# Performance work log

Measured on AMD Instinct MI355X. Metric: run time of the kernel, lower is better.

The kernel has to match this reference:

```python
import jax, jax.numpy as jnp
import numpy as np

N_NODES = 100000
N_EDGES = 400000
B = 1024
D_XD = 78
SEQ = 1000
EMB = 128
HID = 300
NF = 32
OUT_DIM = 128


def setup_inputs():
    key = jax.random.key(0)
    ks = jax.random.split(key, 40)
    rn = lambda k, s, sc=0.05: jax.random.normal(k, s, dtype=jnp.float32) * sc
    inp = {}
    inp['x'] = rn(ks[0], (N_NODES, D_XD), 1.0)
    inp['edge_index'] = jax.random.randint(ks[1], (2, N_EDGES), 0, N_NODES, dtype=jnp.int32)
    inp['batch'] = jnp.sort(jax.random.randint(ks[2], (N_NODES,), 0, B, dtype=jnp.int32))
    inp['target'] = jax.random.randint(ks[3], (B, SEQ), 0, 26, dtype=jnp.int32)
    inp['embs'] = rn(ks[4], (B * 13, 133), 1.0)
    inp['W1'] = rn(ks[5], (D_XD, D_XD)); inp['b1'] = jnp.zeros((D_XD,), jnp.float32)
    inp['W2'] = rn(ks[6], (D_XD, D_XD * 2)); inp['b2'] = jnp.zeros((D_XD * 2,), jnp.float32)
    inp['W3'] = rn(ks[7], (D_XD * 2, D_XD * 4)); inp['b3'] = jnp.zeros((D_XD * 4,), jnp.float32)
    inp['fc_g1_w'] = rn(ks[8], (D_XD * 4, 1024)); inp['fc_g1_b'] = jnp.zeros((1024,), jnp.float32)
    inp['fc_g2_w'] = rn(ks[9], (1024, OUT_DIM)); inp['fc_g2_b'] = jnp.zeros((OUT_DIM,), jnp.float32)
    inp['emb_xt'] = rn(ks[10], (26, EMB), 1.0)
    inp['conv_w'] = rn(ks[11], (NF, SEQ, 8)); inp['conv_b'] = jnp.zeros((NF,), jnp.float32)
    inp['fc1xt_w'] = rn(ks[12], (NF * 121, OUT_DIM)); inp['fc1xt_b'] = jnp.zeros((OUT_DIM,), jnp.float32)
    inp['fg_lin_w'] = rn(ks[13], (133, HID)); inp['fg_lin_b'] = jnp.zeros((HID,), jnp.float32)
    inp['Wq'] = rn(ks[14], (HID, HID)); inp['Wk'] = rn(ks[15], (HID, HID)); inp['Wv'] = rn(ks[16], (HID, HID))
    inp['ln_g'] = jnp.ones((HID,), jnp.float32); inp['ln_b'] = jnp.zeros((HID,), jnp.float32)
    inp['fg_out_w'] = rn(ks[17], (HID, OUT_DIM)); inp['fg_out_b'] = jnp.zeros((OUT_DIM,), jnp.float32)
    inp['fc1_w'] = rn(ks[18], (3 * OUT_DIM, 1024)); inp['fc1_b'] = jnp.zeros((1024,), jnp.float32)
    inp['fc2_w'] = rn(ks[19], (1024, 512)); inp['fc2_b'] = jnp.zeros((512,), jnp.float32)
    inp['out_w'] = rn(ks[20], (512, 1)); inp['out_b'] = jnp.zeros((1,), jnp.float32)
    return inp


def _gcn_conv(h_in, W, b, src, dst, dis):
    # PyG GCNConv: x' = D^-1/2 (A+I) D^-1/2 (X W) + b
    h = h_in @ W
    norm = dis[src] * dis[dst]  # [E]
    agg = jax.ops.segment_sum(h[src] * norm[:, None], dst, num_segments=h.shape[0])
    agg = agg + h * (dis * dis)[:, None]  # self-loop term
    return agg + b


def _forward(x, embs, W1, b1, W2, b2, W3, b3, fc_g1_w, fc_g1_b, fc_g2_w, fc_g2_b,
             emb_xt, conv_w, conv_b, fc1xt_w, fc1xt_b, fg_lin_w, fg_lin_b,
             Wq, Wk, Wv, ln_g, ln_b, fg_out_w, fg_out_b,
             fc1_w, fc1_b, fc2_w, fc2_b, out_w, out_b,
             edge_index, batch, target):
    src, dst = edge_index[0], edge_index[1]
    deg = jax.ops.segment_sum(jnp.ones_like(dst, jnp.float32), dst, num_segments=x.shape[0]) + 1.0
    dis = jax.lax.rsqrt(deg)
    h = jax.nn.relu(_gcn_conv(x, W1, b1, src, dst, dis))
    h = jax.nn.relu(_gcn_conv(h, W2, b2, src, dst, dis))
    h = jax.nn.relu(_gcn_conv(h, W3, b3, src, dst, dis))
    g = jax.ops.segment_max(h, batch, num_segments=B)  # global max pool
    g = jnp.where(jnp.isfinite(g), g, 0.0)
    g = jax.nn.relu(g @ fc_g1_w + fc_g1_b)
    g = g @ fc_g2_w + fc_g2_b  # dropout is identity at eval
    # protein branch: embedding + Conv1d(in=1000, out=32, k=8) over embed axis
    e = emb_xt[target]  # [B, SEQ, EMB]
    c = jax.lax.conv_general_dilated(e, conv_w, (1,), 'VALID',
                                     dimension_numbers=('NCH', 'OIH', 'NCH'))
    c = c + conv_b[None, :, None]  # [B, 32, 121]
    xt = c.reshape(B, NF * 121) @ fc1xt_w + fc1xt_b
    # functional-group prompt branch (KANO-style): linear -> self-attn -> LN -> gather row i*13
    f = (embs @ fg_lin_w + fg_lin_b).reshape(B, 13, HID)
    q = f @ Wq; k = f @ Wk; v = f @ Wv
    attn = jax.nn.softmax(jnp.einsum('bqd,bkd->bqk', q, k) / jnp.sqrt(jnp.float32(HID)), axis=-1)
    f2 = f + jnp.einsum('bqk,bkd->bqd', attn, v)
    mu = f2.mean(-1, keepdims=True)
    var = f2.var(-1, keepdims=True)
    f2 = (f2 - mu) * jax.lax.rsqrt(var + 1e-5) * ln_g + ln_b
    fg = f2[:, 0, :] @ fg_out_w + fg_out_b  # row i*13 per molecule
    xc = jnp.concatenate([g, xt, fg], axis=1)  # [B, 3*OUT_DIM]
    xc = jax.nn.relu(xc @ fc1_w + fc1_b)
    xc = jax.nn.relu(xc @ fc2_w + fc2_b)
    return xc @ out_w + out_b


def reference(x, edge_index, batch, target, embs, W1, b1, W2, b2, W3, b3,
              fc_g1_w, fc_g1_b, fc_g2_w, fc_g2_b, emb_xt, conv_w, conv_b,
              fc1xt_w, fc1xt_b, fg_lin_w, fg_lin_b, Wq, Wk, Wv, ln_g, ln_b,
              fg_out_w, fg_out_b, fc1_w, fc1_b, fc2_w, fc2_b, out_w, out_b):
    return _forward(x, embs, W1, b1, W2, b2, W3, b3, fc_g1_w, fc_g1_b, fc_g2_w, fc_g2_b,
                    emb_xt, conv_w, conv_b, fc1xt_w, fc1xt_b, fg_lin_w, fg_lin_b,
                    Wq, Wk, Wv, ln_g, ln_b, fg_out_w, fg_out_b,
                    fc1_w, fc1_b, fc2_w, fc2_b, out_w, out_b,
                    edge_index, batch, target)
```

## Files before the change

### kernel.cpp

```cpp
#include <hip/hip_runtime.h>
#include <hip/hip_bf16.h>
#include <math.h>

#define NNODES 100000
#define NEDGES 400000
#define NB     1024
#define SEQ    1000
#define HID    300
#define NBLK1  ((NNODES + 255) / 256)

typedef __attribute__((ext_vector_type(8))) short short8;
typedef __attribute__((ext_vector_type(4))) float f32x4;

__device__ __forceinline__ float bf_lo(unsigned int v) { return __uint_as_float(v << 16); }
__device__ __forceinline__ float bf_hi(unsigned int v) { return __uint_as_float(v & 0xffff0000u); }
__device__ __forceinline__ unsigned int bf_pack(float lo, float hi) {
    __hip_bfloat16 a = __float2bfloat16(lo), b = __float2bfloat16(hi);
    unsigned short ua = *(unsigned short*)&a, ub = *(unsigned short*)&b;
    return (unsigned int)ua | ((unsigned int)ub << 16);
}

__global__ void cvt_pad_kernel(const float* __restrict__ in, __hip_bfloat16* __restrict__ out,
                               int M, int K, int Kpad)
{
    long idx = (long)blockIdx.x * 256 + threadIdx.x;
    if (idx >= (long)M * Kpad) return;
    int m = idx / Kpad, k = idx % Kpad;
    out[idx] = __float2bfloat16(k < K ? in[(long)m * K + k] : 0.f);
}

__global__ void transpose_cvt_kernel(const float* __restrict__ in, __hip_bfloat16* __restrict__ out,
                                     int K, int N, int Kpad)
{
    long idx = (long)blockIdx.x * 256 + threadIdx.x;
    if (idx >= (long)N * Kpad) return;
    int n = idx / Kpad, k = idx % Kpad;
    out[idx] = __float2bfloat16(k < K ? in[(long)k * N + n] : 0.f);
}

struct TBatch {
    const float* src[12];
    __hip_bfloat16* dst[12];
    int K[12]; int N[12]; int Kpad[12];
    int bstart[13];
};

__global__ __launch_bounds__(256) void transpose_batch_kernel(TBatch tb)
{
    int blk = blockIdx.x;
    int d = 0;
    while (d < 11 && blk >= tb.bstart[d + 1]) ++d;
    long idx = (long)(blk - tb.bstart[d]) * 256 + threadIdx.x;
    long tot = (long)tb.N[d] * tb.Kpad[d];
    if (idx >= tot) return;
    int Kpad = tb.Kpad[d];
    int n = idx / Kpad, k = idx % Kpad;
    tb.dst[d][idx] = __float2bfloat16(k < tb.K[d] ? tb.src[d][(long)k * tb.N[d] + n] : 0.f);
}

__global__ __launch_bounds__(256) void gemm_bf16_kernel(
    const __hip_bfloat16* __restrict__ A, const __hip_bfloat16* __restrict__ Bt,
    const float* __restrict__ bias, void* __restrict__ C,
    int M, int N, int Kpad, int lda, int ldc, int Npad_out,
    int relu, int outbf, int chunk)
{
    __shared__ __align__(16) __hip_bfloat16 As[64][40];
    __shared__ __align__(16) __hip_bfloat16 Bs[64][40];
    int tid = threadIdx.x;
    int wave = tid >> 6, lane = tid & 63;
    int wm = wave >> 1, wn = wave & 1;
    int quad = lane >> 4, l16 = lane & 15;
    int row0 = blockIdx.y * 64, col0 = blockIdx.x * 64;

    int kbeg = 0, kend = Kpad;
    if (chunk > 0) { kbeg = blockIdx.z * chunk; kend = kbeg + chunk; if (kend > Kpad) kend = Kpad; }

    f32x4 acc[2][2];
    #pragma unroll
    for (int i = 0; i < 2; ++i)
        #pragma unroll
        for (int j = 0; j < 2; ++j) acc[i][j] = (f32x4){0.f, 0.f, 0.f, 0.f};

    int r = tid >> 2, cch = (tid & 3) * 8;

    for (int k0 = kbeg; k0 < kend; k0 += 32) {
        uint4 av = {0u, 0u, 0u, 0u};
        if (row0 + r < M) av = *(const uint4*)(A + (size_t)(row0 + r) * lda + k0 + cch);
        *(uint4*)(&As[r][cch]) = av;
        uint4 bv = {0u, 0u, 0u, 0u};
        if (col0 + r < N) bv = *(const uint4*)(Bt + (size_t)(col0 + r) * Kpad + k0 + cch);
        *(uint4*)(&Bs[r][cch]) = bv;
        __syncthreads();

        short8 a0 = *(const short8*)(&As[wm * 32 + l16][quad * 8]);
        short8 a1 = *(const short8*)(&As[wm * 32 + 16 + l16][quad * 8]);
        short8 b0 = *(const short8*)(&Bs[wn * 32 + l16][quad * 8]);
        short8 b1 = *(const short8*)(&Bs[wn * 32 + 16 + l16][quad * 8]);
        acc[0][0] = __builtin_amdgcn_mfma_f32_16x16x32_bf16(a0, b0, acc[0][0], 0, 0, 0);
        acc[0][1] = __builtin_amdgcn_mfma_f32_16x16x32_bf16(a0, b1, acc[0][1], 0, 0, 0);
        acc[1][0] = __builtin_amdgcn_mfma_f32_16x16x32_bf16(a1, b0, acc[1][0], 0, 0, 0);
        acc[1][1] = __builtin_amdgcn_mfma_f32_16x16x32_bf16(a1, b1, acc[1][1], 0, 0, 0);
        __syncthreads();
    }

    #pragma unroll
    for (int ti = 0; ti < 2; ++ti) {
        int rbase = row0 + wm * 32 + ti * 16 + quad * 4;
        #pragma unroll
        for (int tj = 0; tj < 2; ++tj) {
            int cc = col0 + wn * 32 + tj * 16 + l16;
            if (cc >= Npad_out) continue;
            #pragma unroll
            for (int reg = 0; reg < 4; ++reg) {
                int rr = rbase + reg;
                if (rr >= M) continue;
                float v = acc[ti][tj][reg];
                if (chunk > 0) {
                    if (cc < N) atomicAdd((float*)C + (size_t)rr * ldc + cc, v);
                } else {
                    float ov = 0.f;
                    if (cc < N) {
                        if (bias) v += bias[cc];
                        if (relu) v = fmaxf(v, 0.f);
                        ov = v;
                    }
                    if (outbf) ((__hip_bfloat16*)C)[(size_t)rr * ldc + cc] = __float2bfloat16(ov);
                    else       ((float*)C)[(size_t)rr * ldc + cc] = ov;
                }
            }
        }
    }
}

static void launch_gemm_bf16(const __hip_bfloat16* A, const __hip_bfloat16* Bt, const float* bias,
                             void* C, int M, int N, int Kpad, int lda, int ldc, int Npad_out,
                             int relu, int outbf, int splitz, hipStream_t stream)
{
    int cover = N > Npad_out ? N : Npad_out;
    int chunk = (splitz > 1) ? (Kpad / splitz) : 0;
    dim3 grid((cover + 63) / 64, (M + 63) / 64, splitz > 1 ? splitz : 1);
    gemm_bf16_kernel<<<grid, 256, 0, stream>>>(A, Bt, bias, C, M, N, Kpad, lda, ldc, Npad_out,
                                               relu, outbf, chunk);
}

__global__ __launch_bounds__(256) void gemm_big_kernel(
    const __hip_bfloat16* __restrict__ A, const __hip_bfloat16* __restrict__ Bt,
    const float* __restrict__ bias, __hip_bfloat16* __restrict__ C,
    int M, int N, int Kpad, int lda, int ldc, int Npad_out)
{
    __shared__ __align__(16) __hip_bfloat16 As[128][40];
    __shared__ __align__(16) __hip_bfloat16 Bs[64][40];
    int tid = threadIdx.x;
    int wave = tid >> 6, lane = tid & 63;
    int wm = wave >> 1, wn = wave & 1;
    int quad = lane >> 4, l16 = lane & 15;
    int row0 = blockIdx.y * 128, col0 = blockIdx.x * 64;

    f32x4 acc[4][2];
    #pragma unroll
    for (int i = 0; i < 4; ++i)
        #pragma unroll
        for (int j = 0; j < 2; ++j) acc[i][j] = (f32x4){0.f, 0.f, 0.f, 0.f};

    int r = tid >> 2, cch = (tid & 3) * 8;

    for (int k0 = 0; k0 < Kpad; k0 += 32) {
        uint4 av0 = {0u, 0u, 0u, 0u}, av1 = {0u, 0u, 0u, 0u}, bv = {0u, 0u, 0u, 0u};
        if (row0 + r < M)      av0 = *(const uint4*)(A + (size_t)(row0 + r) * lda + k0 + cch);
        if (row0 + r + 64 < M) av1 = *(const uint4*)(A + (size_t)(row0 + r + 64) * lda + k0 + cch);
        if (col0 + r < N)      bv  = *(const uint4*)(Bt + (size_t)(col0 + r) * Kpad + k0 + cch);
        *(uint4*)(&As[r][cch]) = av0;
        *(uint4*)(&As[r + 64][cch]) = av1;
        *(uint4*)(&Bs[r][cch]) = bv;
        __syncthreads();

        short8 af[4], bféin[2];
        #pragma unroll
        for (int i = 0; i < 4; ++i)
            af[i] = *(const short8*)(&As[wm * 64 + i * 16 + l16][quad * 8]);
        #pragma unroll
        for (int j = 0; j < 2; ++j)
            bféin[j] = *(const short8*)(&Bs[wn * 32 + j * 16 + l16][quad * 8]);
        #pragma unroll
        for (int i = 0; i < 4; ++i)
            #pragma unroll
            for (int j = 0; j < 2; ++j)
                acc[i][j] = __builtin_amdgcn_mfma_f32_16x16x32_bf16(af[i], bféin[j], acc[i][j], 0, 0, 0);
        __syncthreads();
    }

    #pragma unroll
    for (int ti = 0; ti < 4; ++ti) {
        int rbase = row0 + wm * 64 + ti * 16 + quad * 4;
        #pragma unroll
        for (int tj = 0; tj < 2; ++tj) {
            int cc = col0 + wn * 32 + tj * 16 + l16;
            if (cc >= Npad_out) continue;
            #pragma unroll
            for (int reg = 0; reg < 4; ++reg) {
                int rr = rbase + reg;
                if (rr >= M) continue;
                float v = acc[ti][tj][reg];
                float ov = 0.f;
                if (cc < N) ov = fmaxf(v + bias[cc], 0.f);
                C[(size_t)rr * ldc + cc] = __float2bfloat16(ov);
            }
        }
    }
}

static void launch_gemm_big(const __hip_bfloat16* A, const __hip_bfloat16* Bt, const float* bias,
                            __hip_bfloat16* C, int M, int N, int Kpad, int lda, int ldc,
                            int Npad_out, hipStream_t stream)
{
    int cover = N > Npad_out ? N : Npad_out;
    dim3 grid((cover + 63) / 64, (M + 127) / 128);
    gemm_big_kernel<<<grid, 256, 0, stream>>>(A, Bt, bias, C, M, N, Kpad, lda, ldc, Npad_out);
}

__global__ void deg_kernel(const int* __restrict__ dst, int* __restrict__ deg, int E)
{
    int e = blockIdx.x * 256 + threadIdx.x;
    if (e < E) atomicAdd(&deg[dst[e]], 1);
}

__global__ void dis_kernel(const int* __restrict__ deg, float* __restrict__ dis,
                           float* __restrict__ selfc, int n)
{
    int i = blockIdx.x * 256 + threadIdx.x;
    if (i < n) {
        float d = (float)deg[i] + 1.0f;
        float r = 1.0f / sqrtf(d);
        dis[i] = r;
        selfc[i] = r * r;
    }
}

__global__ __launch_bounds__(256) void scan_p1(const int* __restrict__ deg,
                                               int* __restrict__ off, int* __restrict__ bsum)
{
    __shared__ int s[256];
    int tid = threadIdx.x;
    int i = blockIdx.x * 256 + tid;
    int v = (i < NNODES) ? deg[i] : 0;
    s[tid] = v;
    __syncthreads();
    #pragma unroll
    for (int d = 1; d < 256; d <<= 1) {
        int t = (tid >= d) ? s[tid - d] : 0;
        __syncthreads();
        s[tid] += t;
        __syncthreads();
    }
    if (i < NNODES) off[i] = s[tid] - v;
    if (tid == 255) bsum[blockIdx.x] = s[255];
}

__global__ __launch_bounds__(512) void scan_p2(int* __restrict__ bsum)
{
    __shared__ int s[512];
    int tid = threadIdx.x;
    int v = (tid < NBLK1) ? bsum[tid] : 0;
    s[tid] = v;
    __syncthreads();
    #pragma unroll
    for (int d = 1; d < 512; d <<= 1) {
        int t = (tid >= d) ? s[tid - d] : 0;
        __syncthreads();
        s[tid] += t;
        __syncthreads();
    }
    if (tid < NBLK1) bsum[tid] = s[tid] - v;
}

__global__ __launch_bounds__(256) void scan_p3(int* __restrict__ off, const int* __restrict__ bsum,
                                               int* __restrict__ cur)
{
    int i = blockIdx.x * 256 + threadIdx.x;
    if (i < NNODES) {
        int v = off[i] + bsum[blockIdx.x];
        off[i] = v;
        cur[i] = v;
    }
    if (i == NNODES) off[NNODES] = NEDGES;
}

__global__ void fill_csr_kernel(const int* __restrict__ src, const int* __restrict__ dst,
                                const float* __restrict__ dis, int* __restrict__ cur,
                                int* __restrict__ csr_src, float* __restrict__ csr_w, int E)
{
    int e = blockIdx.x * 256 + threadIdx.x;
    if (e >= E) return;
    int s = src[e], d = dst[e];
    int p = atomicAdd(&cur[d], 1);
    csr_src[p] = s;
    csr_w[p] = dis[s] * dis[d];
}

__global__ __launch_bounds__(256) void gcn_agg2(
    const __hip_bfloat16* __restrict__ Tin, const int* __restrict__ off,
    const int* __restrict__ csr_src, const float* __restrict__ csr_w,
    const float* __restrict__ selfc, __hip_bfloat16* __restrict__ out,
    int half, int nc)
{
    int wave = threadIdx.x >> 6, lane = threadIdx.x & 63;
    int node = blockIdx.x * 4 + wave;
    if (node >= NNODES) return;
    const unsigned int* Tp = (const unsigned int*)Tin;
    unsigned int* Op = (unsigned int*)out;
    size_t rb = (size_t)node * half;
    bool m0 = lane < half;
    bool m1 = (nc > 1) && (lane + 64 < half);
    float sc = selfc[node];
    float a0x = 0.f, a0y = 0.f, a1x = 0.f, a1y = 0.f;
    float b0x = 0.f, b0y = 0.f, b1x = 0.f, b1y = 0.f;
    if (m0) { unsigned int v = Tp[rb + lane];      a0x = bf_lo(v) * sc; a0y = bf_hi(v) * sc; }
    if (m1) { unsigned int v = Tp[rb + lane + 64]; a1x = bf_lo(v) * sc; a1y = bf_hi(v) * sc; }
    int s0 = off[node], s1 = off[node + 1];
    int e = s0;
    for (; e + 2 <= s1; e += 2) {
        int i0 = csr_src[e], i1 = csr_src[e + 1];
        float w0 = csr_w[e], w1 = csr_w[e + 1];
        size_t p0 = (size_t)i0 * half, p1 = (size_t)i1 * half;
        unsigned int v00 = 0u, v01 = 0u, v10 = 0u, v11 = 0u;
        if (m0) { v00 = Tp[p0 + lane]; v10 = Tp[p1 + lane]; }
        if (m1) { v01 = Tp[p0 + lane + 64]; v11 = Tp[p1 + lane + 64]; }
        if (m0) {
            a0x += bf_lo(v00) * w0; a0y += bf_hi(v00) * w0;
            b0x += bf_lo(v10) * w1; b0y += bf_hi(v10) * w1;
        }
        if (m1) {
            a1x += bf_lo(v01) * w0; a1y += bf_hi(v01) * w0;
            b1x += bf_lo(v11) * w1; b1y += bf_hi(v11) * w1;
        }
    }
    if (e < s1) {
        int i0 = csr_src[e];
        float w0 = csr_w[e];
        size_t p0 = (size_t)i0 * half;
        if (m0) { unsigned int v = Tp[p0 + lane];      a0x += bf_lo(v) * w0; a0y += bf_hi(v) * w0; }
        if (m1) { unsigned int v = Tp[p0 + lane + 64]; a1x += bf_lo(v) * w0; a1y += bf_hi(v) * w0; }
    }
    if (m0) Op[rb + lane]      = bf_pack(a0x + b0x, a0y + b0y);
    if (m1) Op[rb + lane + 64] = bf_pack(a1x + b1x, a1y + b1y);
}

__global__ __launch_bounds__(256) void pool_max_bf16(
    const __hip_bfloat16* __restrict__ H, const int* __restrict__ batch,
    __hip_bfloat16* __restrict__ g)
{
    int b = blockIdx.x;
    int lo = 0, hi = NNODES;
    while (lo < hi) { int mid = (lo + hi) >> 1; if (batch[mid] < b) lo = mid + 1; else hi = mid; }
    int s = lo;
    hi = NNODES;
    while (lo < hi) { int mid = (lo + hi) >> 1; if (batch[mid] < b + 1) lo = mid + 1; else hi = mid; }
    int e = lo;
    int tid = threadIdx.x;
    if (tid < 160) {
        const unsigned int* Hp = (const unsigned int*)H;
        float mx = 0.f, my = 0.f;
        for (int i = s; i < e; ++i) {
            unsigned int v = Hp[(size_t)i * 160 + tid];
            mx = fmaxf(mx, bf_lo(v));
            my = fmaxf(my, bf_hi(v));
        }
        ((unsigned int*)g)[(size_t)b * 160 + tid] = bf_pack(mx, my);
    }
}

__global__ void conv_transpose_kernel(const float* __restrict__ w, __hip_bfloat16* __restrict__ wt)
{
    int idx = blockIdx.x * 256 + threadIdx.x;
    if (idx >= 256000) return;
    int o = idx / 8000;
    int rem = idx - o * 8000;
    int i = rem >> 3, k = rem & 7;
    wt[i * 256 + o * 8 + k] = __float2bfloat16(w[idx]);
}

__global__ __launch_bounds__(256) void conv_agg_kernel(
    const __hip_bfloat16* __restrict__ cwt, const int* __restrict__ target,
    __hip_bfloat16* __restrict__ aggw)
{
    __shared__ int tb_s[SEQ];
    __shared__ int cnt[26];
    __shared__ int boff[27];
    __shared__ int curs[26];
    __shared__ int bucket[SEQ];
    __shared__ float comb[3][256];
    int b = blockIdx.x, tid = threadIdx.x;
    int wave = tid >> 6, lane = tid & 63;
    const int* tb = target + b * SEQ;
    if (tid < 26) cnt[tid] = 0;
    __syncthreads();
    for (int i = tid; i < SEQ; i += 256) {
        int a = tb[i];
        tb_s[i] = a;
        atomicAdd(&cnt[a], 1);
    }
    __syncthreads();
    if (tid == 0) {
        int run = 0;
        for (int a = 0; a < 26; ++a) { boff[a] = run; curs[a] = run; run += cnt[a]; }
        boff[26] = run;
    }
    __syncthreads();
    for (int i = tid; i < SEQ; i += 256) {
        int a = tb_s[i];
        int p = atomicAdd(&curs[a], 1);
        bucket[p] = i;
    }
    __syncthreads();

    const uint2* cw = (const uint2*)cwt;
    uint2* aw = (uint2*)aggw;
    for (int a = 0; a < 26; ++a) {
        int s = boff[a], e = boff[a + 1];
        float x0 = 0.f, x1 = 0.f, x2 = 0.f, x3 = 0.f;
        float y0 = 0.f, y1 = 0.f, y2 = 0.f, y3 = 0.f;
        int j = s + wave;
        for (; j + 4 < e; j += 8) {
            uint2 v = cw[(size_t)bucket[j] * 64 + lane];
            uint2 u = cw[(size_t)bucket[j + 4] * 64 + lane];
            x0 += bf_lo(v.x); x1 += bf_hi(v.x); x2 += bf_lo(v.y); x3 += bf_hi(v.y);
            y0 += bf_lo(u.x); y1 += bf_hi(u.x); y2 += bf_lo(u.y); y3 += bf_hi(u.y);
        }
        if (j < e) {
            uint2 v = cw[(size_t)bucket[j] * 64 + lane];
            x0 += bf_lo(v.x); x1 += bf_hi(v.x); x2 += bf_lo(v.y); x3 += bf_hi(v.y);
        }
        x0 += y0; x1 += y1; x2 += y2; x3 += y3;
        if (wave > 0) {
            comb[wave - 1][lane * 4 + 0] = x0;
            comb[wave - 1][lane * 4 + 1] = x1;
            comb[wave - 1][lane * 4 + 2] = x2;
            comb[wave - 1][lane * 4 + 3] = x3;
        }
        __syncthreads();
        if (wave == 0) {
            x0 += comb[0][lane * 4 + 0] + comb[1][lane * 4 + 0] + comb[2][lane * 4 + 0];
            x1 += comb[0][lane * 4 + 1] + comb[1][lane * 4 + 1] + comb[2][lane * 4 + 1];
            x2 += comb[0][lane * 4 + 2] + comb[1][lane * 4 + 2] + comb[2][lane * 4 + 2];
            x3 += comb[0][lane * 4 + 3] + comb[1][lane * 4 + 3] + comb[2][lane * 4 + 3];
            uint2 o;
            o.x = bf_pack(x0, x1);
            o.y = bf_pack(x2, x3);
            aw[(size_t)b * 1664 + a * 64 + lane] = o;
        }
        __syncthreads();
    }
}

__global__ __launch_bounds__(128) void conv_wc_kernel(
    const float* __restrict__ emb, const float* __restrict__ w_fc, float* __restrict__ Wc)
{
    int o = blockIdx.x;
    int ak = blockIdx.y;
    int a = ak >> 3, k = ak & 7;
    int j = threadIdx.x;
    const float* wp = w_fc + (long)(o * 121) * 128 + j;
    const float* ep = emb + a * 128 + k;
    float s = 0.f;
    #pragma unroll 11
    for (int t = 0; t < 121; ++t) s += ep[t] * wp[t * 128];
    Wc[(long)(a * 256 + o * 8 + k) * 128 + j] = s;
}

__global__ void xtb_init_kernel(const float* __restrict__ b_fc, float* __restrict__ xtb)
{
    xtb[threadIdx.x] = b_fc[threadIdx.x];
}

__global__ __launch_bounds__(128) void convb_fold_kernel(
    const float* __restrict__ w_fc, const float* __restrict__ conv_b, float* __restrict__ xtb)
{
    int o = blockIdx.x, j = threadIdx.x;
    const float* wp = w_fc + (long)(o * 121) * 128 + j;
    float s = 0.f;
    for (int t = 0; t < 121; ++t) s += wp[t * 128];
    atomicAdd(&xtb[j], s * conv_b[o]);
}

__global__ void xc_convbias_kernel(const float* __restrict__ xtb, float* __restrict__ xc)
{
    int idx = blockIdx.x * 256 + threadIdx.x;
    if (idx >= NB * 128) return;
    int b = idx >> 7, j = idx & 127;
    xc[(long)b * 384 + 128 + j] = xtb[j];
}

__global__ __launch_bounds__(256) void attn_ln_kernel(
    const __hip_bfloat16* __restrict__ Fb, const __hip_bfloat16* __restrict__ Kf,
    const __hip_bfloat16* __restrict__ Vf, const __hip_bfloat16* __restrict__ q0,
    const float* __restrict__ ln_g, const float* __restrict__ ln_b,
    __hip_bfloat16* __restrict__ out)
{
    int b = blockIdx.x, tid = threadIdx.x;
    __shared__ float qs[HID];
    __shared__ float sc[13];
    __shared__ float red[256];
    __shared__ float red2[256];
    __shared__ float rowv[HID];
    __shared__ float mean_s, inv_s;

    for (int d = tid; d < HID; d += 256) qs[d] = __bfloat162float(q0[(size_t)b * 320 + d]);
    __syncthreads();
    if (tid < 208) {
        int k = tid >> 4, sub = tid & 15;
        const __hip_bfloat16* kr = Kf + ((size_t)b * 13 + k) * 320;
        float p = 0.f;
        for (int d = sub; d < HID; d += 16) p += qs[d] * __bfloat162float(kr[d]);
        red[tid] = p;
    }
    __syncthreads();
    if (tid < 208 && (tid & 15) == 0) {
        float s = 0.f;
        #pragma unroll
        for (int j = 0; j < 16; ++j) s += red[tid + j];
        sc[tid >> 4] = s * 0.0577350269189626f;
    }
    __syncthreads();
    if (tid == 0) {
        float mx = sc[0];
        for (int k = 1; k < 13; ++k) mx = fmaxf(mx, sc[k]);
        float ssum = 0.f;
        for (int k = 0; k < 13; ++k) { float e = expf(sc[k] - mx); sc[k] = e; ssum += e; }
        float inv = 1.0f / ssum;
        for (int k = 0; k < 13; ++k) sc[k] *= inv;
    }
    __syncthreads();
    for (int d = tid; d < HID; d += 256) {
        float v = __bfloat162float(Fb[((size_t)b * 13) * 320 + d]);
        #pragma unroll
        for (int k = 0; k < 13; ++k)
            v += sc[k] * __bfloat162float(Vf[((size_t)b * 13 + k) * 320 + d]);
        rowv[d] = v;
    }
    __syncthreads();
    float s1 = 0.f, s2 = 0.f;
    for (int d = tid; d < HID; d += 256) { float v = rowv[d]; s1 += v; s2 += v * v; }
    red[tid] = s1; red2[tid] = s2;
    __syncthreads();
    for (int s = 128; s > 0; s >>= 1) {
        if (tid < s) { red[tid] += red[tid + s]; red2[tid] += red2[tid + s]; }
        __syncthreads();
    }
    if (tid == 0) {
        float mean = red[0] / (float)HID;
        float var = red2[0] / (float)HID - mean * mean;
        mean_s = mean;
        inv_s = 1.0f / sqrtf(var + 1e-5f);
    }
    __syncthreads();
    for (int d = tid; d < 320; d += 256) {
        float v = 0.f;
        if (d < HID) v = (rowv[d] - mean_s) * inv_s * ln_g[d] + ln_b[d];
        out[(size_t)b * 320 + d] = __float2bfloat16(v);
    }
}

__global__ __launch_bounds__(256) void final_out_kernel(
    const float* __restrict__ X, const float* __restrict__ w,
    const float* __restrict__ bias, float* __restrict__ out)
{
    int b = blockIdx.x, tid = threadIdx.x;
    __shared__ float red[256];
    float p = X[(long)b * 512 + tid] * w[tid] + X[(long)b * 512 + tid + 256] * w[tid + 256];
    red[tid] = p;
    __syncthreads();
    for (int s = 128; s > 0; s >>= 1) {
        if (tid < s) red[tid] += red[tid + s];
        __syncthreads();
    }
    if (tid == 0) out[b] = red[0] + bias[0];
}

extern "C" void kernel_launch(void* const* d_in, const int* in_sizes, int n_in,
                              void* d_out, int out_size, void* d_ws, size_t ws_size,
                              hipStream_t stream)
{
    const float* x        = (const float*)d_in[0];
    const int*   ei       = (const int*)d_in[1];
    const int*   batch    = (const int*)d_in[2];
    const int*   target   = (const int*)d_in[3];
    const float* embs     = (const float*)d_in[4];
    const float* W1       = (const float*)d_in[5];
    const float* b1       = (const float*)d_in[6];
    const float* W2       = (const float*)d_in[7];
    const float* b2       = (const float*)d_in[8];
    const float* W3       = (const float*)d_in[9];
    const float* b3       = (const float*)d_in[10];
    const float* fc_g1_w  = (const float*)d_in[11];
    const float* fc_g1_b  = (const float*)d_in[12];
    const float* fc_g2_w  = (const float*)d_in[13];
    const float* fc_g2_b  = (const float*)d_in[14];
    const float* emb_xt   = (const float*)d_in[15];
    const float* conv_w   = (const float*)d_in[16];
    const float* conv_b   = (const float*)d_in[17];
    const float* fc1xt_w  = (const float*)d_in[18];
    const float* fc1xt_b  = (const float*)d_in[19];
    const float* fg_lin_w = (const float*)d_in[20];
    const float* fg_lin_b = (const float*)d_in[21];
    const float* Wq       = (const float*)d_in[22];
    const float* Wk       = (const float*)d_in[23];
    const float* Wv       = (const float*)d_in[24];
    const float* ln_g     = (const float*)d_in[25];
    const float* ln_b     = (const float*)d_in[26];
    const float* fg_out_w = (const float*)d_in[27];
    const float* fg_out_b = (const float*)d_in[28];
    const float* fc1_w    = (const float*)d_in[29];
    const float* fc1_b    = (const float*)d_in[30];
    const float* fc2_w    = (const float*)d_in[31];
    const float* fc2_b    = (const float*)d_in[32];
    const float* out_w    = (const float*)d_in[33];
    const float* out_b    = (const float*)d_in[34];

    const int* src = ei;
    const int* dst = ei + NEDGES;
    typedef __hip_bfloat16 bf;

    char* p = (char*)d_ws;
    auto alloc = [&](size_t bytes) { char* r = p; p += (bytes + 255) & ~(size_t)255; return r; };
    bf*   xb      = (bf*)alloc((size_t)NNODES * 96 * 2);
    bf*   T       = (bf*)alloc((size_t)NNODES * 160 * 2);
    bf*   H       = (bf*)alloc((size_t)NNODES * 320 * 2);
    int*  deg     = (int*)alloc(NNODES * 4);
    float* dis    = (float*)alloc(NNODES * 4);
    float* selfc  = (float*)alloc(NNODES * 4);
    int*  off     = (int*)alloc((NNODES + 1) * 4);
    int*  bsum    = (int*)alloc(512 * 4);
    int*  csr_src = (int*)alloc(NEDGES * 4);
    float* csr_w  = (float*)alloc(NEDGES * 4);
    bf*   w1t     = (bf*)alloc(78 * 96 * 2);
    bf*   w2t     = (bf*)alloc(156 * 96 * 2);
    bf*   w3t     = (bf*)alloc(312 * 160 * 2);
    bf*   fcg1t   = (bf*)alloc(1024 * 320 * 2);
    bf*   fcg2t   = (bf*)alloc(128 * 1024 * 2);
    bf*   fglint  = (bf*)alloc(300 * 160 * 2);
    bf*   wkt     = (bf*)alloc(300 * 320 * 2);
    bf*   wvt     = (bf*)alloc(300 * 320 * 2);
    bf*   wqt     = (bf*)alloc(300 * 320 * 2);
    bf*   fgoutt  = (bf*)alloc(128 * 320 * 2);
    bf*   fc1t    = (bf*)alloc(1024 * 384 * 2);
    bf*   fc2t    = (bf*)alloc(512 * 1024 * 2);
    bf*   g       = (bf*)alloc((size_t)NB * 320 * 2);
    bf*   G1b     = (bf*)alloc((size_t)NB * 1024 * 2);
    bf*   embsb   = (bf*)alloc((size_t)NB * 13 * 160 * 2);
    bf*   Fbuf    = (bf*)alloc((size_t)NB * 13 * 320 * 2);
    bf*   Kbuf    = (bf*)alloc((size_t)NB * 13 * 320 * 2);
    bf*   Vbuf    = (bf*)alloc((size_t)NB * 13 * 320 * 2);
    bf*   Qbuf    = (bf*)alloc((size_t)NB * 320 * 2);
    bf*   f2row   = (bf*)alloc((size_t)NB * 320 * 2);
    float* xc     = (float*)alloc((size_t)NB * 384 * 4);
    bf*   xcb     = (bf*)alloc((size_t)NB * 384 * 2);
    float* F2     = (float*)alloc((size_t)NB * 512 * 4);
    bf*   cwt     = (bf*)alloc(256000 * 2);
    bf*   aggwb   = (bf*)alloc((size_t)NB * 6656 * 2);
    float* Wc     = (float*)alloc((size_t)6656 * 128 * 4);
    bf*   Wct     = (bf*)alloc((size_t)128 * 6656 * 2);
    float* xtb    = (float*)alloc(128 * 4);

    hipMemsetAsync(deg, 0, NNODES * sizeof(int), stream);
    deg_kernel<<<(NEDGES + 255) / 256, 256, 0, stream>>>(dst, deg, NEDGES);
    dis_kernel<<<(NNODES + 255) / 256, 256, 0, stream>>>(deg, dis, selfc, NNODES);
    scan_p1<<<NBLK1, 256, 0, stream>>>(deg, off, bsum);
    scan_p2<<<1, 512, 0, stream>>>(bsum);
    scan_p3<<<NBLK1, 256, 0, stream>>>(off, bsum, deg);
    fill_csr_kernel<<<(NEDGES + 255) / 256, 256, 0, stream>>>(src, dst, dis, deg, csr_src, csr_w, NEDGES);

    {
        TBatch tb;
        const float* srcs[12] = {W1, W2, W3, fc_g1_w, fc_g2_w, fg_lin_w, Wk, Wv, Wq, fg_out_w, fc1_w, fc2_w};
        bf* dsts[12]          = {w1t, w2t, w3t, fcg1t, fcg2t, fglint, wkt, wvt, wqt, fgoutt, fc1t, fc2t};
        int Ks[12]    = {78, 78, 156, 312, 1024, 133, 300, 300, 300, 300, 384, 1024};
        int Ns[12]    = {78, 156, 312, 1024, 128, 300, 300, 300, 300, 128, 1024, 512};
        int Kpads[12] = {96, 96, 160, 320, 1024, 160, 320, 320, 320, 320, 384, 1024};
        int bs = 0;
        for (int i = 0; i < 12; ++i) {
            tb.src[i] = srcs[i]; tb.dst[i] = dsts[i];
            tb.K[i] = Ks[i]; tb.N[i] = Ns[i]; tb.Kpad[i] = Kpads[i];
            tb.bstart[i] = bs;
            bs += (int)(((long)Ns[i] * Kpads[i] + 255) / 256);
        }
        tb.bstart[12] = bs;
        transpose_batch_kernel<<<bs, 256, 0, stream>>>(tb);
    }
    cvt_pad_kernel<<<((long)NNODES * 96 + 255) / 256, 256, 0, stream>>>(x, xb, NNODES, 78, 96);
    cvt_pad_kernel<<<((long)NB * 13 * 160 + 255) / 256, 256, 0, stream>>>(embs, embsb, NB * 13, 133, 160);

    int agrid = (NNODES + 3) / 4;
    gcn_agg2<<<agrid, 256, 0, stream>>>(xb, off, csr_src, csr_w, selfc, T, 48, 1);
    launch_gemm_big(T, w1t, b1, H, NNODES, 78, 96, 96, 96, 96, stream);

    gcn_agg2<<<agrid, 256, 0, stream>>>(H, off, csr_src, csr_w, selfc, T, 48, 1);
    launch_gemm_big(T, w2t, b2, H, NNODES, 156, 96, 96, 160, 160, stream);

    gcn_agg2<<<agrid, 256, 0, stream>>>(H, off, csr_src, csr_w, selfc, T, 80, 2);
    launch_gemm_big(T, w3t, b3, H, NNODES, 312, 160, 160, 320, 320, stream);

    pool_max_bf16<<<NB, 256, 0, stream>>>(H, batch, g);
    launch_gemm_bf16(g, fcg1t, fc_g1_b, G1b, NB, 1024, 320, 320, 1024, 1024, 1, 1, 1, stream);
    launch_gemm_bf16(G1b, fcg2t, fc_g2_b, xc, NB, 128, 1024, 1024, 384, 128, 0, 0, 1, stream);

    conv_transpose_kernel<<<(256000 + 255) / 256, 256, 0, stream>>>(conv_w, cwt);
    conv_agg_kernel<<<NB, 256, 0, stream>>>(cwt, target, aggwb);
    conv_wc_kernel<<<dim3(32, 208), 128, 0, stream>>>(emb_xt, fc1xt_w, Wc);
    transpose_cvt_kernel<<<((long)128 * 6656 + 255) / 256, 256, 0, stream>>>(Wc, Wct, 6656, 128, 6656);
    xtb_init_kernel<<<1, 128, 0, stream>>>(fc1xt_b, xtb);
    convb_fold_kernel<<<32, 128, 0, stream>>>(fc1xt_w, conv_b, xtb);
    xc_convbias_kernel<<<(NB * 128 + 255) / 256, 256, 0, stream>>>(xtb, xc);
    launch_gemm_bf16(aggwb, Wct, nullptr, xc + 128, NB, 128, 6656, 6656, 384, 128, 0, 0, 8, stream);

    launch_gemm_bf16(embsb, fglint, fg_lin_b, Fbuf, NB * 13, 300, 160, 160, 320, 320, 0, 1, 1, stream);
    launch_gemm_bf16(Fbuf, wkt, nullptr, Kbuf, NB * 13, 300, 320, 320, 320, 320, 0, 1, 1, stream);
    launch_gemm_bf16(Fbuf, wvt, nullptr, Vbuf, NB * 13, 300, 320, 320, 320, 320, 0, 1, 1, stream);
    launch_gemm_bf16(Fbuf, wqt, nullptr, Qbuf, NB, 300, 320, 13 * 320, 320, 320, 0, 1, 1, stream);
    attn_ln_kernel<<<NB, 256, 0, stream>>>(Fbuf, Kbuf, Vbuf, Qbuf, ln_g, ln_b, f2row);
    launch_gemm_bf16(f2row, fgoutt, fg_out_b, xc + 256, NB, 128, 320, 320, 384, 128, 0, 0, 1, stream);

    cvt_pad_kernel<<<((long)NB * 384 + 255) / 256, 256, 0, stream>>>(xc, xcb, NB, 384, 384);
    launch_gemm_bf16(xcb, fc1t, fc1_b, G1b, NB, 1024, 384, 384, 1024, 1024, 1, 1, 1, stream);
    launch_gemm_bf16(G1b, fc2t, fc2_b, F2, NB, 512, 1024, 1024, 512, 512, 1, 0, 1, stream);
    final_out_kernel<<<NB, 256, 0, stream>>>(F2, out_w, out_b, (float*)d_out);
}
```

Measured before the change: 760.0 us.

## Fold fg_lin into Q/K/V weights, add strip GEMM, unroll GCN aggregation

Three separate changes. First, the fg_lin weight is precomposed with Wq, Wk and Wv, and the bias is folded in, so Q, K and V are computed directly from the 160-wide embeddings instead of chaining off the 320-wide F. Second, the GCN dense layers get a new strip GEMM that loads a 128-row A tile into LDS once and loops over every output column tile, reading B from global memory. Third, the edge aggregation loop is unrolled by four with four accumulator sets to raise memory-level parallelism. This adds small weight-precompose GEMMs to every call, rounds the composed weights to bf16, and may lower occupancy because of the large LDS tile.

```diff
diff --git a/kernel.cpp b/kernel.cpp
--- a/kernel.cpp
+++ b/kernel.cpp
@@ -56,6 +56,16 @@
     int Kpad = tb.Kpad[d];
     int n = idx / Kpad, k = idx % Kpad;
     tb.dst[d][idx] = __float2bfloat16(k < tb.K[d] ? tb.src[d][(long)k * tb.N[d] + n] : 0.f);
+}
+
+__global__ void bias_fold_kernel(const float* __restrict__ b, const float* __restrict__ W,
+                                 float* __restrict__ out, int K, int N)
+{
+    int n = blockIdx.x * 256 + threadIdx.x;
+    if (n >= N) return;
+    float s = 0.f;
+    for (int k = 0; k < K; ++k) s += b[k] * W[(size_t)k * N + n];
+    out[n] = s;
 }
 
 __global__ __launch_bounds__(256) void gemm_bf16_kernel(
@@ -143,10 +153,10 @@
                                                relu, outbf, chunk);
 }
 
-__global__ __launch_bounds__(256) void gemm_big_kernel(
+__global__ __launch_bounds__(256) void gemm_mt_kernel(
     const __hip_bfloat16* __restrict__ A, const __hip_bfloat16* __restrict__ Bt,
     const float* __restrict__ bias, __hip_bfloat16* __restrict__ C,
-    int M, int N, int Kpad, int lda, int ldc, int Npad_out)
+    int M, int N, int Kpad, int lda, int ldc, int Npad_out, int relu)
 {
     __shared__ __align__(16) __hip_bfloat16 As[128][40];
     __shared__ __align__(16) __hip_bfloat16 Bs[64][40];
@@ -174,18 +184,18 @@
         *(uint4*)(&Bs[r][cch]) = bv;
         __syncthreads();
 
-        short8 af[4], bféin[2];
+        short8 af[4], bfr[2];
         #pragma unroll
         for (int i = 0; i < 4; ++i)
             af[i] = *(const short8*)(&As[wm * 64 + i * 16 + l16][quad * 8]);
         #pragma unroll
         for (int j = 0; j < 2; ++j)
-            bféin[j] = *(const short8*)(&Bs[wn * 32 + j * 16 + l16][quad * 8]);
+            bfr[j] = *(const short8*)(&Bs[wn * 32 + j * 16 + l16][quad * 8]);
         #pragma unroll
         for (int i = 0; i < 4; ++i)
             #pragma unroll
             for (int j = 0; j < 2; ++j)
-                acc[i][j] = __builtin_amdgcn_mfma_f32_16x16x32_bf16(af[i], bféin[j], acc[i][j], 0, 0, 0);
+                acc[i][j] = __builtin_amdgcn_mfma_f32_16x16x32_bf16(af[i], bfr[j], acc[i][j], 0, 0, 0);
         __syncthreads();
     }
 
@@ -202,20 +212,100 @@
                 if (rr >= M) continue;
                 float v = acc[ti][tj][reg];
                 float ov = 0.f;
-                if (cc < N) ov = fmaxf(v + bias[cc], 0.f);
+                if (cc < N) {
+                    if (bias) v += bias[cc];
+                    if (relu) v = fmaxf(v, 0.f);
+                    ov = v;
+                }
                 C[(size_t)rr * ldc + cc] = __float2bfloat16(ov);
             }
         }
     }
 }
 
-static void launch_gemm_big(const __hip_bfloat16* A, const __hip_bfloat16* Bt, const float* bias,
-                            __hip_bfloat16* C, int M, int N, int Kpad, int lda, int ldc,
-                            int Npad_out, hipStream_t stream)
+static void launch_gemm_mt(const __hip_bfloat16* A, const __hip_bfloat16* Bt, const float* bias,
+                           __hip_bfloat16* C, int M, int N, int Kpad, int lda, int ldc,
+                           int Npad_out, int relu, hipStream_t stream)
 {
     int cover = N > Npad_out ? N : Npad_out;
     dim3 grid((cover + 63) / 64, (M + 127) / 128);
-    gemm_big_kernel<<<grid, 256, 0, stream>>>(A, Bt, bias, C, M, N, Kpad, lda, ldc, Npad_out);
+    gemm_mt_kernel<<<grid, 256, 0, stream>>>(A, Bt, bias, C, M, N, Kpad, lda, ldc, Npad_out, relu);
+}
+
+__global__ __launch_bounds__(256) void gemm_strip_kernel(
+    const __hip_bfloat16* __restrict__ A, const __hip_bfloat16* __restrict__ Bt,
+    const float* __restrict__ bias, __hip_bfloat16* __restrict__ C,
+    int M, int N, int Kpad, int lda, int ldc, int Npad_out)
+{
+    __shared__ __align__(16) __hip_bfloat16 As[128][168];
+    int tid = threadIdx.x;
+    int wave = tid >> 6, lane = tid & 63;
+    int wm = wave >> 1, wn = wave & 1;
+    int quad = lane >> 4, l16 = lane & 15;
+    int row0 = blockIdx.x * 128;
+
+    int nch = Kpad >> 3;
+    for (int idx = tid; idx < 128 * nch; idx += 256) {
+        int rr = idx / nch, ch = idx - rr * nch;
+        uint4 v = {0u, 0u, 0u, 0u};
+        if (row0 + rr < M) v = *(const uint4*)(A + (size_t)(row0 + rr) * lda + ch * 8);
+        *(uint4*)(&As[rr][ch * 8]) = v;
+    }
+    __syncthreads();
+
+    const short8 bz = {0, 0, 0, 0, 0, 0, 0, 0};
+    int nct = (Npad_out + 63) >> 6;
+    for (int ct = 0; ct < nct; ++ct) {
+        int col0 = ct * 64;
+        f32x4 acc[4][2];
+        #pragma unroll
+        for (int i = 0; i < 4; ++i)
+            #pragma unroll
+            for (int j = 0; j < 2; ++j) acc[i][j] = (f32x4){0.f, 0.f, 0.f, 0.f};
+
+        for (int k0 = 0; k0 < Kpad; k0 += 32) {
+            short8 af[4], bfr[2];
+            #pragma unroll
+            for (int i = 0; i < 4; ++i)
+                af[i] = *(const short8*)(&As[wm * 64 + i * 16 + l16][k0 + quad * 8]);
+            #pragma unroll
+            for (int j = 0; j < 2; ++j) {
+                int cb = col0 + wn * 32 + j * 16 + l16;
+                bfr[j] = (cb < N) ? *(const short8*)(Bt + (size_t)cb * Kpad + k0 + quad * 8) : bz;
+            }
+            #pragma unroll
+            for (int i = 0; i < 4; ++i)
+                #pragma unroll
+                for (int j = 0; j < 2; ++j)
+                    acc[i][j] = __builtin_amdgcn_mfma_f32_16x16x32_bf16(af[i], bfr[j], acc[i][j], 0, 0, 0);
+        }
+
+        #pragma unroll
+        for (int ti = 0; ti < 4; ++ti) {
+            int rbase = row0 + wm * 64 + ti * 16 + quad * 4;
+            #pragma unroll
+            for (int tj = 0; tj < 2; ++tj) {
+                int cc = col0 + wn * 32 + tj * 16 + l16;
+                if (cc >= Npad_out) continue;
+                #pragma unroll
+                for (int reg = 0; reg < 4; ++reg) {
+                    int rr = rbase + reg;
+                    if (rr >= M) continue;
+                    float ov = 0.f;
+                    if (cc < N) ov = fmaxf(acc[ti][tj][reg] + bias[cc], 0.f);
+                    C[(size_t)rr * ldc + cc] = __float2bfloat16(ov);
+                }
+            }
+        }
+    }
+}
+
+static void launch_gemm_strip(const __hip_bfloat16* A, const __hip_bfloat16* Bt, const float* bias,
+                              __hip_bfloat16* C, int M, int N, int Kpad, int lda, int ldc,
+                              int Npad_out, hipStream_t stream)
+{
+    dim3 grid((M + 127) / 128);
+    gemm_strip_kernel<<<grid, 256, 0, stream>>>(A, Bt, bias, C, M, N, Kpad, lda, ldc, Npad_out);
 }
 
 __global__ void deg_kernel(const int* __restrict__ dst, int* __restrict__ deg, int E)
@@ -314,24 +404,47 @@
     float sc = selfc[node];
     float a0x = 0.f, a0y = 0.f, a1x = 0.f, a1y = 0.f;
     float b0x = 0.f, b0y = 0.f, b1x = 0.f, b1y = 0.f;
+    float c0x = 0.f, c0y = 0.f, c1x = 0.f, c1y = 0.f;
+    float d0x = 0.f, d0y = 0.f, d1x = 0.f, d1y = 0.f;
     if (m0) { unsigned int v = Tp[rb + lane];      a0x = bf_lo(v) * sc; a0y = bf_hi(v) * sc; }
     if (m1) { unsigned int v = Tp[rb + lane + 64]; a1x = bf_lo(v) * sc; a1y = bf_hi(v) * sc; }
     int s0 = off[node], s1 = off[node + 1];
     int e = s0;
+    for (; e + 4 <= s1; e += 4) {
+        int i0 = csr_src[e], i1 = csr_src[e + 1], i2 = csr_src[e + 2], i3 = csr_src[e + 3];
+        float w0 = csr_w[e], w1 = csr_w[e + 1], w2 = csr_w[e + 2], w3 = csr_w[e + 3];
+        size_t p0 = (size_t)i0 * half, p1 = (size_t)i1 * half;
+        size_t p2 = (size_t)i2 * half, p3 = (size_t)i3 * half;
+        if (m0) {
+            unsigned int v0 = Tp[p0 + lane], v1 = Tp[p1 + lane];
+            unsigned int v2 = Tp[p2 + lane], v3 = Tp[p3 + lane];
+            a0x += bf_lo(v0) * w0; a0y += bf_hi(v0) * w0;
+            b0x += bf_lo(v1) * w1; b0y += bf_hi(v1) * w1;
+            c0x += bf_lo(v2) * w2; c0y += bf_hi(v2) * w2;
+            d0x += bf_lo(v3) * w3; d0y += bf_hi(v3) * w3;
+        }
+        if (m1) {
+            unsigned int v0 = Tp[p0 + lane + 64], v1 = Tp[p1 + lane + 64];
+            unsigned int v2 = Tp[p2 + lane + 64], v3 = Tp[p3 + lane + 64];
+            a1x += bf_lo(v0) * w0; a1y += bf_hi(v0) * w0;
+            b1x += bf_lo(v1) * w1; b1y += bf_hi(v1) * w1;
+            c1x += bf_lo(v2) * w2; c1y += bf_hi(v2) * w2;
+            d1x += bf_lo(v3) * w3; d1y += bf_hi(v3) * w3;
+        }
+    }
     for (; e + 2 <= s1; e += 2) {
         int i0 = csr_src[e], i1 = csr_src[e + 1];
         float w0 = csr_w[e], w1 = csr_w[e + 1];
         size_t p0 = (size_t)i0 * half, p1 = (size_t)i1 * half;
-        unsigned int v00 = 0u, v01 = 0u, v10 = 0u, v11 = 0u;
-        if (m0) { v00 = Tp[p0 + lane]; v10 = Tp[p1 + lane]; }
-        if (m1) { v01 = Tp[p0 + lane + 64]; v11 = Tp[p1 + lane + 64]; }
         if (m0) {
-            a0x += bf_lo(v00) * w0; a0y += bf_hi(v00) * w0;
-            b0x += bf_lo(v10) * w1; b0y += bf_hi(v10) * w1;
+            unsigned int v0 = Tp[p0 + lane], v1 = Tp[p1 + lane];
+            a0x += bf_lo(v0) * w0; a0y += bf_hi(v0) * w0;
+            b0x += bf_lo(v1) * w1; b0y += bf_hi(v1) * w1;
         }
         if (m1) {
-            a1x += bf_lo(v01) * w0; a1y += bf_hi(v01) * w0;
-            b1x += bf_lo(v11) * w1; b1y += bf_hi(v11) * w1;
+            unsigned int v0 = Tp[p0 + lane + 64], v1 = Tp[p1 + lane + 64];
+            a1x += bf_lo(v0) * w0; a1y += bf_hi(v0) * w0;
+            b1x += bf_lo(v1) * w1; b1y += bf_hi(v1) * w1;
         }
     }
     if (e < s1) {
@@ -341,8 +454,8 @@
         if (m0) { unsigned int v = Tp[p0 + lane];      a0x += bf_lo(v) * w0; a0y += bf_hi(v) * w0; }
         if (m1) { unsigned int v = Tp[p0 + lane + 64]; a1x += bf_lo(v) * w0; a1y += bf_hi(v) * w0; }
     }
-    if (m0) Op[rb + lane]      = bf_pack(a0x + b0x, a0y + b0y);
-    if (m1) Op[rb + lane + 64] = bf_pack(a1x + b1x, a1y + b1y);
+    if (m0) Op[rb + lane]      = bf_pack((a0x + b0x) + (c0x + d0x), (a0y + b0y) + (c0y + d0y));
+    if (m1) Op[rb + lane + 64] = bf_pack((a1x + b1x) + (c1x + d1x), (a1y + b1y) + (c1y + d1y));
 }
 
 __global__ __launch_bounds__(256) void pool_max_bf16(
@@ -644,6 +757,13 @@
     bf*   fgoutt  = (bf*)alloc(128 * 320 * 2);
     bf*   fc1t    = (bf*)alloc(1024 * 384 * 2);
     bf*   fc2t    = (bf*)alloc(512 * 1024 * 2);
+    bf*   fglwb   = (bf*)alloc(133 * 320 * 2);
+    bf*   wk2t    = (bf*)alloc(300 * 160 * 2);
+    bf*   wv2t    = (bf*)alloc(300 * 160 * 2);
+    bf*   wq2t    = (bf*)alloc(300 * 160 * 2);
+    float* bk2    = (float*)alloc(300 * 4);
+    float* bv2    = (float*)alloc(300 * 4);
+    float* bq2    = (float*)alloc(300 * 4);
     bf*   g       = (bf*)alloc((size_t)NB * 320 * 2);
     bf*   G1b     = (bf*)alloc((size_t)NB * 1024 * 2);
     bf*   embsb   = (bf*)alloc((size_t)NB * 13 * 160 * 2);
@@ -691,13 +811,13 @@
 
     int agrid = (NNODES + 3) / 4;
     gcn_agg2<<<agrid, 256, 0, stream>>>(xb, off, csr_src, csr_w, selfc, T, 48, 1);
-    launch_gemm_big(T, w1t, b1, H, NNODES, 78, 96, 96, 96, 96, stream);
+    launch_gemm_strip(T, w1t, b1, H, NNODES, 78, 96, 96, 96, 96, stream);
 
     gcn_agg2<<<agrid, 256, 0, stream>>>(H, off, csr_src, csr_w, selfc, T, 48, 1);
-    launch_gemm_big(T, w2t, b2, H, NNODES, 156, 96, 96, 160, 160, stream);
+    launch_gemm_strip(T, w2t, b2, H, NNODES, 156, 96, 96, 160, 160, stream);
 
     gcn_agg2<<<agrid, 256, 0, stream>>>(H, off, csr_src, csr_w, selfc, T, 80, 2);
-    launch_gemm_big(T, w3t, b3, H, NNODES, 312, 160, 160, 320, 320, stream);
+    launch_gemm_strip(T, w3t, b3, H, NNODES, 312, 160, 160, 320, 320, stream);
 
     pool_max_bf16<<<NB, 256, 0, stream>>>(H, batch, g);
     launch_gemm_bf16(g, fcg1t, fc_g1_b, G1b, NB, 1024, 320, 320, 1024, 1024, 1, 1, 1, stream);
@@ -712,10 +832,17 @@
     xc_convbias_kernel<<<(NB * 128 + 255) / 256, 256, 0, stream>>>(xtb, xc);
     launch_gemm_bf16(aggwb, Wct, nullptr, xc + 128, NB, 128, 6656, 6656, 384, 128, 0, 0, 8, stream);
 
-    launch_gemm_bf16(embsb, fglint, fg_lin_b, Fbuf, NB * 13, 300, 160, 160, 320, 320, 0, 1, 1, stream);
-    launch_gemm_bf16(Fbuf, wkt, nullptr, Kbuf, NB * 13, 300, 320, 320, 320, 320, 0, 1, 1, stream);
-    launch_gemm_bf16(Fbuf, wvt, nullptr, Vbuf, NB * 13, 300, 320, 320, 320, 320, 0, 1, 1, stream);
-    launch_gemm_bf16(Fbuf, wqt, nullptr, Qbuf, NB, 300, 320, 13 * 320, 320, 320, 0, 1, 1, stream);
+    cvt_pad_kernel<<<(133 * 320 + 255) / 256, 256, 0, stream>>>(fg_lin_w, fglwb, 133, 300, 320);
+    launch_gemm_bf16(wkt, fglwb, nullptr, wk2t, 300, 133, 320, 320, 160, 160, 0, 1, 1, stream);
+    launch_gemm_bf16(wvt, fglwb, nullptr, wv2t, 300, 133, 320, 320, 160, 160, 0, 1, 1, stream);
+    launch_gemm_bf16(wqt, fglwb, nullptr, wq2t, 300, 133, 320, 320, 160, 160, 0, 1, 1, stream);
+    bias_fold_kernel<<<2, 256, 0, stream>>>(fg_lin_b, Wk, bk2, 300, 300);
+    bias_fold_kernel<<<2, 256, 0, stream>>>(fg_lin_b, Wv, bv2, 300, 300);
+    bias_fold_kernel<<<2, 256, 0, stream>>>(fg_lin_b, Wq, bq2, 300, 300);
+    launch_gemm_mt(embsb, fglint, fg_lin_b, Fbuf, NB * 13, 300, 160, 160, 320, 320, 0, stream);
+    launch_gemm_mt(embsb, wk2t, bk2, Kbuf, NB * 13, 300, 160, 160, 320, 320, 0, stream);
+    launch_gemm_mt(embsb, wv2t, bv2, Vbuf, NB * 13, 300, 160, 160, 320, 320, 0, stream);
+    launch_gemm_bf16(embsb, wq2t, bq2, Qbuf, NB, 300, 160, 13 * 160, 320, 320, 0, 1, 1, stream);
     attn_ln_kernel<<<NB, 256, 0, stream>>>(Fbuf, Kbuf, Vbuf, Qbuf, ln_g, ln_b, f2row);
     launch_gemm_bf16(f2row, fgoutt, fg_out_b, xc + 256, NB, 128, 320, 320, 384, 128, 0, 0, 1, stream);
 
```

Measured after the change: 1.029 ms. 35.5% more time.
